# Performance work log

Hardware: AMD Instinct MI355X
Metric: run time of the kernel (lower is better)

Reference implementation:

```python
import jax, jax.numpy as jnp
import numpy as np

B, S, D = 32, 4096, 512   # batch, seq_len, input_dim
A, K = 3, 4               # attractor_dim, num_attractors
OUT = 512                 # output_dim


def setup_inputs() -> dict:
    key = jax.random.key(0)
    ks = jax.random.split(key, 10)
    s = 0.02
    return {
        "x": jax.random.normal(ks[0], (B, S, D), dtype=jnp.float32),
        "centers": jax.random.normal(ks[1], (K, A), dtype=jnp.float32),
        "Wa": jax.random.normal(ks[2], (D, A), dtype=jnp.float32) * s,
        "ba": jnp.zeros((A,), dtype=jnp.float32),
        "Wh": jax.random.normal(ks[3], (A, 2 * A), dtype=jnp.float32) * 0.5,
        "bh": jnp.zeros((2 * A,), dtype=jnp.float32),
        "Wk": jax.random.normal(ks[4], (2 * A, K), dtype=jnp.float32) * 0.5,
        "bk": jnp.zeros((K,), dtype=jnp.float32),
        "Wout": jax.random.normal(ks[5], (K * D, OUT), dtype=jnp.float32) * s,
        "bout": jnp.zeros((OUT,), dtype=jnp.float32),
    }


def reference(x, centers, Wa, ba, Wh, bh, Wk, bk, Wout, bout):
    # project to attractor space: [B,S,A]
    af = jnp.einsum("bsd,da->bsa", x, Wa) + ba
    # L2 distance to each attractor center: [B,S,K]
    diff = af[:, :, :, None] - centers.T[None, None, :, :]   # [B,S,A,K]
    distances = jnp.sqrt(jnp.sum(diff * diff, axis=2))
    # tiny MLP weights (batched over all timesteps at once): [B,S,K]
    base = jax.nn.relu(af @ Wh + bh) @ Wk + bk
    distance_weights = jax.nn.softmax(-distances, axis=-1)
    final_weights = jax.nn.softmax(base + distance_weights, axis=-1)
    # attractor-weighted pooling over time, concatenated attractor-major: [B, K*D]
    pooled = jnp.einsum("bsk,bsd->bkd", final_weights, x).reshape(x.shape[0], -1)
    return pooled @ Wout + bout
```

## Files before the change

kernel.cpp:

```cpp
#include <hip/hip_runtime.h>
#include <cstdint>
#include <cstddef>

#define BB 32
#define SS 4096
#define DD 512
#define AA 3
#define KK 4
#define OUTD 512

#define NCHUNK 32
#define ROWS_PER_BLOCK (SS / NCHUNK)
#define ROWS_PER_WAVE  (ROWS_PER_BLOCK / 4)
#define TILE 8
#define NTILES (ROWS_PER_WAVE / TILE)

__global__ __launch_bounds__(256) void fused_pool_kernel(
    const float* __restrict__ x, const float* __restrict__ centers,
    const float* __restrict__ Wa, const float* __restrict__ ba,
    const float* __restrict__ Wh, const float* __restrict__ bh,
    const float* __restrict__ Wk, const float* __restrict__ bk,
    float* __restrict__ pooled)
{
    __shared__ float  sw[68];
    __shared__ float  wa_lds[DD * AA];
    __shared__ float4 fw_lds[4 * TILE];
    __shared__ float  red[4 * 2048];

    const int tid  = threadIdx.x;
    const int wave = tid >> 6;
    const int lane = tid & 63;
    const int b     = blockIdx.y;
    const int chunk = blockIdx.x;

    if (tid < 12)      sw[tid] = centers[tid];
    else if (tid < 15) sw[tid] = ba[tid - 12];
    else if (tid < 33) sw[tid] = Wh[tid - 15];
    else if (tid < 39) sw[tid] = bh[tid - 33];
    else if (tid < 63) sw[tid] = Wk[tid - 39];
    else if (tid < 67) sw[tid] = bk[tid - 63];
    #pragma unroll
    for (int i = 0; i < 6; ++i)
        wa_lds[tid * 6 + i] = Wa[tid * 6 + i];
    for (int i = tid; i < 4 * 2048; i += 256)
        red[i] = 0.0f;
    __syncthreads();

    const int d0 = lane * 8;
    const int s_base = chunk * ROWS_PER_BLOCK + wave * ROWS_PER_WAVE;
    const float* xb = x + (size_t)b * SS * DD + d0;

    #pragma unroll 1
    for (int t = 0; t < NTILES; ++t) {
        const int s0 = s_base + t * TILE;

        {
            float wa[24];
            const float4* wsrc = (const float4*)(wa_lds + d0 * 3);
            #pragma unroll
            for (int i = 0; i < 6; ++i)
                ((float4*)wa)[i] = wsrc[i];

            #pragma unroll 1
            for (int r = 0; r < TILE; ++r) {
                const float* xr = xb + (size_t)(s0 + r) * DD;
                float4 x0 = ((const float4*)xr)[0];
                float4 x1 = ((const float4*)xr)[1];
                float xa[8] = {x0.x, x0.y, x0.z, x0.w, x1.x, x1.y, x1.z, x1.w};

                float p0 = 0.f, p1 = 0.f, p2 = 0.f;
                #pragma unroll
                for (int j = 0; j < 8; ++j) {
                    p0 += xa[j] * wa[j * 3 + 0];
                    p1 += xa[j] * wa[j * 3 + 1];
                    p2 += xa[j] * wa[j * 3 + 2];
                }
                #pragma unroll
                for (int off = 32; off >= 1; off >>= 1) {
                    p0 += __shfl_xor(p0, off, 64);
                    p1 += __shfl_xor(p1, off, 64);
                    p2 += __shfl_xor(p2, off, 64);
                }
                const float af0 = p0 + sw[12];
                const float af1 = p1 + sw[13];
                const float af2 = p2 + sw[14];

                float dist[KK];
                #pragma unroll
                for (int k = 0; k < KK; ++k) {
                    float da = af0 - sw[k * 3 + 0];
                    float db = af1 - sw[k * 3 + 1];
                    float dc = af2 - sw[k * 3 + 2];
                    dist[k] = sqrtf(da * da + db * db + dc * dc);
                }
                float mn = fminf(fminf(dist[0], dist[1]), fminf(dist[2], dist[3]));
                float e[KK]; float esum = 0.f;
                #pragma unroll
                for (int k = 0; k < KK; ++k) { e[k] = __expf(mn - dist[k]); esum += e[k]; }
                const float einv = 1.0f / esum;

                float h[6];
                #pragma unroll
                for (int i6 = 0; i6 < 6; ++i6) {
                    float v = af0 * sw[15 + i6] + af1 * sw[21 + i6]
                            + af2 * sw[27 + i6] + sw[33 + i6];
                    h[i6] = fmaxf(v, 0.0f);
                }
                float logit[KK];
                #pragma unroll
                for (int k = 0; k < KK; ++k) {
                    float v = sw[63 + k];
                    #pragma unroll
                    for (int i6 = 0; i6 < 6; ++i6) v += h[i6] * sw[39 + i6 * 4 + k];
                    logit[k] = v + e[k] * einv;
                }
                float mx = fmaxf(fmaxf(logit[0], logit[1]), fmaxf(logit[2], logit[3]));
                float f0 = __expf(logit[0] - mx), f1 = __expf(logit[1] - mx);
                float f2 = __expf(logit[2] - mx), f3 = __expf(logit[3] - mx);
                const float finv = 1.0f / (f0 + f1 + f2 + f3);

                if (lane == 0) {
                    float4 fwv = {f0 * finv, f1 * finv, f2 * finv, f3 * finv};
                    fw_lds[wave * TILE + r] = fwv;
                }
            }
        }

        {
            float acc[KK][8];
            #pragma unroll
            for (int k = 0; k < KK; ++k)
                #pragma unroll
                for (int j = 0; j < 8; ++j) acc[k][j] = 0.0f;

            #pragma unroll 2
            for (int r = 0; r < TILE; ++r) {
                const float* xr = xb + (size_t)(s0 + r) * DD;
                float4 x0 = ((const float4*)xr)[0];
                float4 x1 = ((const float4*)xr)[1];
                float xa[8] = {x0.x, x0.y, x0.z, x0.w, x1.x, x1.y, x1.z, x1.w};
                float4 fwv = fw_lds[wave * TILE + r];

                #pragma unroll
                for (int j = 0; j < 8; ++j) {
                    acc[0][j] += fwv.x * xa[j];
                    acc[1][j] += fwv.y * xa[j];
                    acc[2][j] += fwv.z * xa[j];
                    acc[3][j] += fwv.w * xa[j];
                }
            }

            float* rw = red + wave * 2048;
            #pragma unroll
            for (int k = 0; k < KK; ++k)
                #pragma unroll
                for (int j = 0; j < 8; ++j)
                    rw[k * 512 + d0 + j] += acc[k][j];
        }
    }

    __syncthreads();

    float* pb = pooled + (size_t)b * (KK * DD);
    for (int c = tid; c < 2048; c += 256) {
        float s = red[c] + red[2048 + c] + red[4096 + c] + red[6144 + c];
        unsafeAtomicAdd(&pb[c], s);
    }
}

__global__ __launch_bounds__(256) void out_gemm_kernel(
    const float* __restrict__ pooled, const float* __restrict__ Wout,
    const float* __restrict__ bout, float* __restrict__ out)
{
    __shared__ float p_sh[128];
    const int tid = threadIdx.x;
    const int cc = blockIdx.x, b = blockIdx.y, jc = blockIdx.z;

    if (tid < 128) p_sh[tid] = pooled[b * 2048 + jc * 128 + tid];
    __syncthreads();

    const int col = cc * 256 + tid;
    const float* wp = Wout + (size_t)(jc * 128) * OUTD + col;
    float acc = 0.f;
    #pragma unroll 8
    for (int jj = 0; jj < 128; ++jj) {
        acc += p_sh[jj] * wp[(size_t)jj * OUTD];
    }
    if (jc == 0) acc += bout[col];
    unsafeAtomicAdd(&out[b * OUTD + col], acc);
}

extern "C" void kernel_launch(void* const* d_in, const int* in_sizes, int n_in,
                              void* d_out, int out_size, void* d_ws, size_t ws_size,
                              hipStream_t stream) {
    (void)in_sizes; (void)n_in; (void)out_size; (void)ws_size;
    const float* x       = (const float*)d_in[0];
    const float* centers = (const float*)d_in[1];
    const float* Wa      = (const float*)d_in[2];
    const float* ba      = (const float*)d_in[3];
    const float* Wh      = (const float*)d_in[4];
    const float* bh      = (const float*)d_in[5];
    const float* Wk      = (const float*)d_in[6];
    const float* bk      = (const float*)d_in[7];
    const float* Wout    = (const float*)d_in[8];
    const float* bout    = (const float*)d_in[9];
    float* out    = (float*)d_out;
    float* pooled = (float*)d_ws;

    hipMemsetAsync(pooled, 0, (size_t)BB * KK * DD * sizeof(float), stream);
    hipMemsetAsync(out, 0, (size_t)BB * OUTD * sizeof(float), stream);

    fused_pool_kernel<<<dim3(NCHUNK, BB), 256, 0, stream>>>(
        x, centers, Wa, ba, Wh, bh, Wk, bk, pooled);
    out_gemm_kernel<<<dim3(2, BB, 16), 256, 0, stream>>>(pooled, Wout, bout, out);
}
```

Before: 429.1 us.

## Split projection across lane groups, keep pooling accumulators in registers

Each wave now processes 8 rows at once for the attractor projection. 8-lane groups each handle one row with coalesced float4 loads, using a transposed Wa in LDS and a 3-step shuffle reduction, in place of one row at a time with a full 64-lane reduction. Pooling accumulators persist in registers across all tiles and are merged once through LDS atomics into a single 2048-float buffer, which removes the per-tile LDS read-modify-write. Chunks per batch double to 64 to give more blocks. In exchange there are more global atomics into pooled and some redundant softmax arithmetic per lane group.

```diff
diff --git a/kernel.cpp b/kernel.cpp
--- a/kernel.cpp
+++ b/kernel.cpp
@@ -9,11 +9,11 @@
 #define KK 4
 #define OUTD 512
 
-#define NCHUNK 32
+#define NCHUNK 64
 #define ROWS_PER_BLOCK (SS / NCHUNK)
 #define ROWS_PER_WAVE  (ROWS_PER_BLOCK / 4)
-#define TILE 8
-#define NTILES (ROWS_PER_WAVE / TILE)
+#define GROUPS 8
+#define NITER (ROWS_PER_WAVE / GROUPS)
 
 __global__ __launch_bounds__(256) void fused_pool_kernel(
     const float* __restrict__ x, const float* __restrict__ centers,
@@ -23,13 +23,15 @@
     float* __restrict__ pooled)
 {
     __shared__ float  sw[68];
-    __shared__ float  wa_lds[DD * AA];
-    __shared__ float4 fw_lds[4 * TILE];
-    __shared__ float  red[4 * 2048];
+    __shared__ float  waT[AA * DD];
+    __shared__ float4 fw_lds[4 * GROUPS];
+    __shared__ float  red[KK * DD];
 
     const int tid  = threadIdx.x;
     const int wave = tid >> 6;
     const int lane = tid & 63;
+    const int g    = lane >> 3;
+    const int c    = lane & 7;
     const int b     = blockIdx.y;
     const int chunk = blockIdx.x;
 
@@ -39,133 +41,127 @@
     else if (tid < 39) sw[tid] = bh[tid - 33];
     else if (tid < 63) sw[tid] = Wk[tid - 39];
     else if (tid < 67) sw[tid] = bk[tid - 63];
+    for (int i = tid; i < AA * DD; i += 256) {
+        int d = i / 3, a = i - 3 * d;
+        waT[a * DD + d] = Wa[i];
+    }
+    for (int i = tid; i < KK * DD; i += 256) red[i] = 0.0f;
+    __syncthreads();
+
+    const int s_base = chunk * ROWS_PER_BLOCK + wave * ROWS_PER_WAVE;
+    const float* xbase = x + (size_t)b * SS * DD;
+
+    float acc[KK][8];
     #pragma unroll
-    for (int i = 0; i < 6; ++i)
-        wa_lds[tid * 6 + i] = Wa[tid * 6 + i];
-    for (int i = tid; i < 4 * 2048; i += 256)
-        red[i] = 0.0f;
-    __syncthreads();
-
-    const int d0 = lane * 8;
-    const int s_base = chunk * ROWS_PER_BLOCK + wave * ROWS_PER_WAVE;
-    const float* xb = x + (size_t)b * SS * DD + d0;
+    for (int k = 0; k < KK; ++k)
+        #pragma unroll
+        for (int j = 0; j < 8; ++j) acc[k][j] = 0.0f;
 
     #pragma unroll 1
-    for (int t = 0; t < NTILES; ++t) {
-        const int s0 = s_base + t * TILE;
+    for (int t = 0; t < NITER; ++t) {
+        const int s0 = s_base + t * GROUPS;
 
         {
-            float wa[24];
-            const float4* wsrc = (const float4*)(wa_lds + d0 * 3);
-            #pragma unroll
-            for (int i = 0; i < 6; ++i)
-                ((float4*)wa)[i] = wsrc[i];
-
-            #pragma unroll 1
-            for (int r = 0; r < TILE; ++r) {
-                const float* xr = xb + (size_t)(s0 + r) * DD;
-                float4 x0 = ((const float4*)xr)[0];
-                float4 x1 = ((const float4*)xr)[1];
-                float xa[8] = {x0.x, x0.y, x0.z, x0.w, x1.x, x1.y, x1.z, x1.w};
-
-                float p0 = 0.f, p1 = 0.f, p2 = 0.f;
+            const float* xg = xbase + (size_t)(s0 + g) * DD + c * 4;
+            float p0 = 0.f, p1 = 0.f, p2 = 0.f;
+            #pragma unroll 4
+            for (int m = 0; m < 16; ++m) {
+                const int d = m * 32;
+                float4 xv = *(const float4*)(xg + d);
+                float4 w0 = *(const float4*)(waT + 0 * DD + d + c * 4);
+                float4 w1 = *(const float4*)(waT + 1 * DD + d + c * 4);
+                float4 w2 = *(const float4*)(waT + 2 * DD + d + c * 4);
+                p0 += xv.x * w0.x + xv.y * w0.y + xv.z * w0.z + xv.w * w0.w;
+                p1 += xv.x * w1.x + xv.y * w1.y + xv.z * w1.z + xv.w * w1.w;
+                p2 += xv.x * w2.x + xv.y * w2.y + xv.z * w2.z + xv.w * w2.w;
+            }
+            #pragma unroll
+            for (int off = 1; off <= 4; off <<= 1) {
+                p0 += __shfl_xor(p0, off, 64);
+                p1 += __shfl_xor(p1, off, 64);
+                p2 += __shfl_xor(p2, off, 64);
+            }
+            const float af0 = p0 + sw[12];
+            const float af1 = p1 + sw[13];
+            const float af2 = p2 + sw[14];
+
+            float dist[KK];
+            #pragma unroll
+            for (int k = 0; k < KK; ++k) {
+                float da = af0 - sw[k * 3 + 0];
+                float db = af1 - sw[k * 3 + 1];
+                float dc = af2 - sw[k * 3 + 2];
+                dist[k] = sqrtf(da * da + db * db + dc * dc);
+            }
+            float mn = fminf(fminf(dist[0], dist[1]), fminf(dist[2], dist[3]));
+            float e[KK]; float esum = 0.f;
+            #pragma unroll
+            for (int k = 0; k < KK; ++k) { e[k] = __expf(mn - dist[k]); esum += e[k]; }
+            const float einv = 1.0f / esum;
+
+            float h[6];
+            #pragma unroll
+            for (int i6 = 0; i6 < 6; ++i6) {
+                float v = af0 * sw[15 + i6] + af1 * sw[21 + i6]
+                        + af2 * sw[27 + i6] + sw[33 + i6];
+                h[i6] = fmaxf(v, 0.0f);
+            }
+            float logit[KK];
+            #pragma unroll
+            for (int k = 0; k < KK; ++k) {
+                float v = sw[63 + k];
                 #pragma unroll
-                for (int j = 0; j < 8; ++j) {
-                    p0 += xa[j] * wa[j * 3 + 0];
-                    p1 += xa[j] * wa[j * 3 + 1];
-                    p2 += xa[j] * wa[j * 3 + 2];
-                }
-                #pragma unroll
-                for (int off = 32; off >= 1; off >>= 1) {
-                    p0 += __shfl_xor(p0, off, 64);
-                    p1 += __shfl_xor(p1, off, 64);
-                    p2 += __shfl_xor(p2, off, 64);
-                }
-                const float af0 = p0 + sw[12];
-                const float af1 = p1 + sw[13];
-                const float af2 = p2 + sw[14];
-
-                float dist[KK];
+                for (int i6 = 0; i6 < 6; ++i6) v += h[i6] * sw[39 + i6 * 4 + k];
+                logit[k] = v + e[k] * einv;
+            }
+            float mx = fmaxf(fmaxf(logit[0], logit[1]), fmaxf(logit[2], logit[3]));
+            float f0 = __expf(logit[0] - mx), f1 = __expf(logit[1] - mx);
+            float f2 = __expf(logit[2] - mx), f3 = __expf(logit[3] - mx);
+            const float finv = 1.0f / (f0 + f1 + f2 + f3);
+            if (c == 0) {
+                float4 fwv = {f0 * finv, f1 * finv, f2 * finv, f3 * finv};
+                fw_lds[wave * GROUPS + g] = fwv;
+            }
+        }
+
+        {
+            const float* xp = xbase + (size_t)s0 * DD;
+            #pragma unroll 2
+            for (int gg = 0; gg < GROUPS; ++gg) {
+                const float* xr = xp + (size_t)gg * DD;
+                float4 xlo = *(const float4*)(xr + 4 * lane);
+                float4 xhi = *(const float4*)(xr + 256 + 4 * lane);
+                float4 fwv = fw_lds[wave * GROUPS + gg];
+                const float fk[KK] = {fwv.x, fwv.y, fwv.z, fwv.w};
                 #pragma unroll
                 for (int k = 0; k < KK; ++k) {
-                    float da = af0 - sw[k * 3 + 0];
-                    float db = af1 - sw[k * 3 + 1];
-                    float dc = af2 - sw[k * 3 + 2];
-                    dist[k] = sqrtf(da * da + db * db + dc * dc);
+                    acc[k][0] += fk[k] * xlo.x;
+                    acc[k][1] += fk[k] * xlo.y;
+                    acc[k][2] += fk[k] * xlo.z;
+                    acc[k][3] += fk[k] * xlo.w;
+                    acc[k][4] += fk[k] * xhi.x;
+                    acc[k][5] += fk[k] * xhi.y;
+                    acc[k][6] += fk[k] * xhi.z;
+                    acc[k][7] += fk[k] * xhi.w;
                 }
-                float mn = fminf(fminf(dist[0], dist[1]), fminf(dist[2], dist[3]));
-                float e[KK]; float esum = 0.f;
-                #pragma unroll
-                for (int k = 0; k < KK; ++k) { e[k] = __expf(mn - dist[k]); esum += e[k]; }
-                const float einv = 1.0f / esum;
-
-                float h[6];
-                #pragma unroll
-                for (int i6 = 0; i6 < 6; ++i6) {
-                    float v = af0 * sw[15 + i6] + af1 * sw[21 + i6]
-                            + af2 * sw[27 + i6] + sw[33 + i6];
-                    h[i6] = fmaxf(v, 0.0f);
-                }
-                float logit[KK];
-                #pragma unroll
-                for (int k = 0; k < KK; ++k) {
-                    float v = sw[63 + k];
-                    #pragma unroll
-                    for (int i6 = 0; i6 < 6; ++i6) v += h[i6] * sw[39 + i6 * 4 + k];
-                    logit[k] = v + e[k] * einv;
-                }
-                float mx = fmaxf(fmaxf(logit[0], logit[1]), fmaxf(logit[2], logit[3]));
-                float f0 = __expf(logit[0] - mx), f1 = __expf(logit[1] - mx);
-                float f2 = __expf(logit[2] - mx), f3 = __expf(logit[3] - mx);
-                const float finv = 1.0f / (f0 + f1 + f2 + f3);
-
-                if (lane == 0) {
-                    float4 fwv = {f0 * finv, f1 * finv, f2 * finv, f3 * finv};
-                    fw_lds[wave * TILE + r] = fwv;
-                }
             }
         }
-
-        {
-            float acc[KK][8];
-            #pragma unroll
-            for (int k = 0; k < KK; ++k)
-                #pragma unroll
-                for (int j = 0; j < 8; ++j) acc[k][j] = 0.0f;
-
-            #pragma unroll 2
-            for (int r = 0; r < TILE; ++r) {
-                const float* xr = xb + (size_t)(s0 + r) * DD;
-                float4 x0 = ((const float4*)xr)[0];
-                float4 x1 = ((const float4*)xr)[1];
-                float xa[8] = {x0.x, x0.y, x0.z, x0.w, x1.x, x1.y, x1.z, x1.w};
-                float4 fwv = fw_lds[wave * TILE + r];
-
-                #pragma unroll
-                for (int j = 0; j < 8; ++j) {
-                    acc[0][j] += fwv.x * xa[j];
-                    acc[1][j] += fwv.y * xa[j];
-                    acc[2][j] += fwv.z * xa[j];
-                    acc[3][j] += fwv.w * xa[j];
-                }
-            }
-
-            float* rw = red + wave * 2048;
-            #pragma unroll
-            for (int k = 0; k < KK; ++k)
-                #pragma unroll
-                for (int j = 0; j < 8; ++j)
-                    rw[k * 512 + d0 + j] += acc[k][j];
-        }
-    }
-
+    }
+
+    #pragma unroll
+    for (int k = 0; k < KK; ++k) {
+        #pragma unroll
+        for (int j = 0; j < 4; ++j)
+            atomicAdd(&red[k * DD + 4 * lane + j], acc[k][j]);
+        #pragma unroll
+        for (int j = 0; j < 4; ++j)
+            atomicAdd(&red[k * DD + 256 + 4 * lane + j], acc[k][4 + j]);
+    }
     __syncthreads();
 
     float* pb = pooled + (size_t)b * (KK * DD);
-    for (int c = tid; c < 2048; c += 256) {
-        float s = red[c] + red[2048 + c] + red[4096 + c] + red[6144 + c];
-        unsafeAtomicAdd(&pb[c], s);
-    }
+    for (int cc2 = tid; cc2 < KK * DD; cc2 += 256)
+        unsafeAtomicAdd(&pb[cc2], red[cc2]);
 }
 
 __global__ __launch_bounds__(256) void out_gemm_kernel(
```

Measured after the change: 505.9 us. 17.9% more time.
